# Performance work log

Measured on AMD Instinct MI355X. Metric: run time of the kernel, lower is better.

## Reference

```python
import jax, jax.numpy as jnp
import numpy as np

B, T, C, H = 4, 2048, 1024, 128

def setup_inputs() -> dict:
    key = jax.random.key(0)
    k1, k2, k3, k4 = jax.random.split(key, 4)
    x = jax.random.normal(k1, (B, T, C), dtype=jnp.float32)
    # nn.Linear(C, H, bias=False) weights, stored as [C, H] so y = x @ W
    scale = 1.0 / np.sqrt(C)
    Wq = jax.random.normal(k2, (C, H), dtype=jnp.float32) * scale
    Wk = jax.random.normal(k3, (C, H), dtype=jnp.float32) * scale
    Wv = jax.random.normal(k4, (C, H), dtype=jnp.float32) * scale
    mask = jnp.tril(jnp.ones((T, T), dtype=jnp.int32))  # causal mask
    return {"x": x, "Wq": Wq, "Wk": Wk, "Wv": Wv, "mask": mask}

def reference(x, Wq, Wk, Wv, mask):
    # x: [B,T,C]; projections to [B,T,H]
    q = jnp.einsum("btc,ch->bth", x, Wq)
    k = jnp.einsum("btc,ch->bth", x, Wk)
    v = jnp.einsum("btc,ch->bth", x, Wv)
    # NOTE: original scales by C**-0.5 (embedding dim), not head_size**-0.5
    inv_scale = x.shape[-1] ** (-0.5)
    scores = jnp.einsum("bth,bsh->bts", q, k) * inv_scale  # [B,T,T]
    scores = jnp.where(mask == 0, -jnp.inf, scores)
    weights = jax.nn.softmax(scores, axis=-1)
    # Dropout(0.1) is identity in eval mode
    return jnp.einsum("bts,bsh->bth", weights, v)  # [B,T,H]
```

## Files before the change

### kernel.cpp

```cpp
#include <hip/hip_runtime.h>
#include <hip/hip_bf16.h>
#include <cstdint>


typedef __bf16 bf16_t;
typedef __bf16 bf16x4 __attribute__((ext_vector_type(4)));
typedef __bf16 bf16x8 __attribute__((ext_vector_type(8)));
typedef float f32x4 __attribute__((ext_vector_type(4)));

#define MFMA16(a, b, c) __builtin_amdgcn_mfma_f32_16x16x32_bf16(a, b, c, 0, 0, 0)

constexpr int T = 2048;
constexpr int C = 1024;
constexpr int H = 128;
constexpr int BK = 64;

__device__ inline void gld16(const void* g, void* l) {
    __builtin_amdgcn_global_load_lds(
        (const __attribute__((address_space(1))) unsigned int*)g,
        (__attribute__((address_space(3))) unsigned int*)l, 16, 0, 0);
}

__global__ __launch_bounds__(256) void transpose_w(const float* __restrict__ Wq,
                                                   const float* __restrict__ Wk,
                                                   const float* __restrict__ Wv,
                                                   bf16_t* __restrict__ Wt) {
    __shared__ bf16_t tile[32][34];
    const int tid = threadIdx.x, blk = blockIdx.x;
    const int z = blk >> 7, rem = blk & 127;
    const int c0 = (rem & 31) * 32, h0 = (rem >> 5) * 32;
    const float* W = z == 0 ? Wq : (z == 1 ? Wk : Wv);
    const int tx = tid & 31, ty = tid >> 5;
#pragma unroll
    for (int i = 0; i < 4; i++)
        tile[ty + 8 * i][tx] = (bf16_t)W[(size_t)(c0 + ty + 8 * i) * H + h0 + tx];
    __syncthreads();
    bf16_t* Wtz = Wt + (size_t)z * H * C;
#pragma unroll
    for (int i = 0; i < 4; i++)
        Wtz[(size_t)(h0 + ty + 8 * i) * C + c0 + tx] = tile[tx][ty + 8 * i];
}

__global__ __launch_bounds__(256) void proj_gemm(const float* __restrict__ x,
                                                 const bf16_t* __restrict__ Wt,
                                                 bf16_t* __restrict__ qout,
                                                 bf16_t* __restrict__ kout,
                                                 bf16_t* __restrict__ vtout) {
    __shared__ __align__(16) float Ab[2][64 * BK];
    __shared__ __align__(16) bf16_t Bb[2][128 * BK];
    const int tid = threadIdx.x;
    const int w = tid >> 6, lane = tid & 63;
    const int m16 = lane & 15, g = lane >> 4;
    const int wm = w & 1, wn = w >> 1;
    const int z = blockIdx.y;
    const int m0 = blockIdx.x * 64;
    const bf16_t* Bsrc = Wt + (size_t)z * H * C;

    auto stage = [&](int s, int k0) {
#pragma unroll
        for (int i = 0; i < 4; i++) {
            const int e = i * 256 + tid;
            const int r = e >> 4, v = e & 15, c4 = v ^ (r & 15);
            gld16(x + (size_t)(m0 + r) * C + k0 + c4 * 4, &Ab[s][(i * 4 + w) * 256]);
        }
#pragma unroll
        for (int i = 0; i < 4; i++) {
            const int e = i * 256 + tid;
            const int r = e >> 3, v = e & 7, c8 = v ^ (r & 7);
            gld16(Bsrc + (size_t)r * C + k0 + c8 * 8, &Bb[s][(i * 4 + w) * 512]);
        }
    };

    f32x4 zero = {0.f, 0.f, 0.f, 0.f};
    f32x4 acc[2][4];
#pragma unroll
    for (int mf = 0; mf < 2; mf++)
#pragma unroll
        for (int nf = 0; nf < 4; nf++) acc[mf][nf] = zero;

    stage(0, 0);
    for (int c = 0; c < C / BK; c++) {
        __syncthreads();
        if (c + 1 < C / BK) stage((c + 1) & 1, (c + 1) * BK);
        const int s = c & 1;

        bf16x8 af[2][2], bfr[4][2];
#pragma unroll
        for (int mf = 0; mf < 2; mf++)
#pragma unroll
            for (int kf = 0; kf < 2; kf++) {
                const int r = wm * 32 + mf * 16 + m16;
                const int c4 = kf * 8 + g * 2;
                const int va = c4 ^ (r & 15), vb = (c4 + 1) ^ (r & 15);
                float4 fa = *(const float4*)(&Ab[s][r * BK + va * 4]);
                float4 fb = *(const float4*)(&Ab[s][r * BK + vb * 4]);
                bf16x8 t;
                t[0] = (bf16_t)fa.x; t[1] = (bf16_t)fa.y;
                t[2] = (bf16_t)fa.z; t[3] = (bf16_t)fa.w;
                t[4] = (bf16_t)fb.x; t[5] = (bf16_t)fb.y;
                t[6] = (bf16_t)fb.z; t[7] = (bf16_t)fb.w;
                af[mf][kf] = t;
            }
#pragma unroll
        for (int nf = 0; nf < 4; nf++)
#pragma unroll
            for (int kf = 0; kf < 2; kf++) {
                const int r = wn * 64 + nf * 16 + m16;
                const int v = (kf * 4 + g) ^ (r & 7);
                bfr[nf][kf] = *(const bf16x8*)(&Bb[s][r * BK + v * 8]);
            }
#pragma unroll
        for (int kf = 0; kf < 2; kf++)
#pragma unroll
            for (int mf = 0; mf < 2; mf++)
#pragma unroll
                for (int nf = 0; nf < 4; nf++)
                    acc[mf][nf] = MFMA16(af[mf][kf], bfr[nf][kf], acc[mf][nf]);
    }

    const float sc = (z == 0) ? 0.03125f : 1.0f;
    if (z < 2) {
        bf16_t* o = (z == 0) ? qout : kout;
#pragma unroll
        for (int mf = 0; mf < 2; mf++)
#pragma unroll
            for (int nf = 0; nf < 4; nf++)
#pragma unroll
                for (int ri = 0; ri < 4; ri++) {
                    const int r = m0 + wm * 32 + mf * 16 + g * 4 + ri;
                    const int n = wn * 64 + nf * 16 + m16;
                    o[(size_t)r * H + n] = (bf16_t)(acc[mf][nf][ri] * sc);
                }
    } else {
#pragma unroll
        for (int mf = 0; mf < 2; mf++) {
            const int t0 = m0 + wm * 32 + mf * 16 + g * 4;
            const int bidx = t0 >> 11, tt = t0 & (T - 1);
#pragma unroll
            for (int nf = 0; nf < 4; nf++) {
                const int h = wn * 64 + nf * 16 + m16;
                bf16x4 vv;
#pragma unroll
                for (int ri = 0; ri < 4; ri++) vv[ri] = (bf16_t)acc[mf][nf][ri];
                *(bf16x4*)(vtout + ((size_t)bidx * H + h) * T + tt) = vv;
            }
        }
    }
}

__global__ __launch_bounds__(512, 4) void attn(const bf16_t* __restrict__ q,
                                               const bf16_t* __restrict__ k,
                                               const bf16_t* __restrict__ vt,
                                               float* __restrict__ out) {
    __shared__ float buf[4][16][128];
    __shared__ __align__(16) bf16_t pbuf[8][16][40];
    __shared__ float mred[8][16], lred[8][16];
    const int tid = threadIdx.x;
    const int w = tid >> 6;
    const int lane = tid & 63;
    const int m16 = lane & 15, g = lane >> 4;
    const int b = blockIdx.x & 3;
    const int kk = blockIdx.x >> 2;
    const int qt = (kk < 64) ? kk : 191 - kk;
    const int q0 = qt * 16;

    const bf16_t* qb = q + (size_t)b * T * H;
    const bf16_t* kb = k + (size_t)b * T * H;
    const bf16_t* vb = vt + (size_t)b * H * T;

    bf16x8 aq[4];
#pragma unroll
    for (int c = 0; c < 4; c++)
        aq[c] = *(const bf16x8*)(qb + (size_t)(q0 + m16) * H + c * 32 + g * 8);

    bf16x8 ones;
#pragma unroll
    for (int i = 0; i < 8; i++) ones[i] = (bf16_t)1.0f;

    f32x4 zero = {0.f, 0.f, 0.f, 0.f};
    f32x4 acc[9];
#pragma unroll
    for (int ht = 0; ht < 9; ht++) acc[ht] = zero;
    float mst[4];
#pragma unroll
    for (int ri = 0; ri < 4; ri++) mst[ri] = -1e30f;

    const int kv_end = q0 + 16;
    bf16x8 kc[8], kn[8], vc[8];
    int kv0 = w * 32;
    if (kv0 < kv_end) {
#pragma unroll
        for (int t = 0; t < 2; t++)
#pragma unroll
            for (int c = 0; c < 4; c++)
                kc[t * 4 + c] = *(const bf16x8*)(kb + (size_t)(kv0 + t * 16 + m16) * H + c * 32 + g * 8);
    }

    for (; kv0 < kv_end; kv0 += 256) {
        f32x4 s[2];
        s[0] = zero; s[1] = zero;
#pragma unroll
        for (int t = 0; t < 2; t++)
#pragma unroll
            for (int c = 0; c < 4; c++)
                s[t] = MFMA16(aq[c], kc[t * 4 + c], s[t]);

#pragma unroll
        for (int ht = 0; ht < 8; ht++)
            vc[ht] = *(const bf16x8*)(vb + (size_t)(ht * 16 + m16) * T + kv0 + g * 8);

        const int kvn = kv0 + 256;
        if (kvn < kv_end) {
#pragma unroll
            for (int t = 0; t < 2; t++)
#pragma unroll
                for (int c = 0; c < 4; c++)
                    kn[t * 4 + c] = *(const bf16x8*)(kb + (size_t)(kvn + t * 16 + m16) * H + c * 32 + g * 8);
        }

        float p0v[4], p1v[4];
#pragma unroll
        for (int ri = 0; ri < 4; ri++) {
            const int row = q0 + g * 4 + ri;
            float v0 = s[0][ri];
            float v1 = s[1][ri];
            if (kv0 + m16 > row) v0 = -1e30f;
            if (kv0 + 16 + m16 > row) v1 = -1e30f;
            float rm = fmaxf(v0, v1);
#pragma unroll
            for (int off = 1; off < 16; off <<= 1) rm = fmaxf(rm, __shfl_xor(rm, off));
            const float mnew = fmaxf(mst[ri], rm);
            const float alpha = __expf(mst[ri] - mnew);
            mst[ri] = mnew;
            p0v[ri] = __expf(v0 - mnew);
            p1v[ri] = __expf(v1 - mnew);
#pragma unroll
            for (int ht = 0; ht < 9; ht++) acc[ht][ri] *= alpha;
        }

#pragma unroll
        for (int ri = 0; ri < 4; ri++) {
            pbuf[w][g * 4 + ri][m16] = (bf16_t)p0v[ri];
            pbuf[w][g * 4 + ri][16 + m16] = (bf16_t)p1v[ri];
        }
        bf16x8 ap = *(const bf16x8*)(&pbuf[w][m16][g * 8]);

#pragma unroll
        for (int ht = 0; ht < 8; ht++)
            acc[ht] = MFMA16(ap, vc[ht], acc[ht]);
        acc[8] = MFMA16(ap, ones, acc[8]);

#pragma unroll
        for (int i = 0; i < 8; i++) kc[i] = kn[i];
    }

    if (m16 == 0) {
#pragma unroll
        for (int ri = 0; ri < 4; ri++) mred[w][g * 4 + ri] = mst[ri];
    }
    __syncthreads();
    float scale[4];
#pragma unroll
    for (int ri = 0; ri < 4; ri++) {
        const int row = g * 4 + ri;
        float mt = mred[0][row];
#pragma unroll
        for (int j = 1; j < 8; j++) mt = fmaxf(mt, mred[j][row]);
        scale[ri] = __expf(mst[ri] - mt);
    }
    if (m16 == 0) {
#pragma unroll
        for (int ri = 0; ri < 4; ri++) lred[w][g * 4 + ri] = acc[8][ri] * scale[ri];
    }
#pragma unroll
    for (int ht = 0; ht < 8; ht++)
#pragma unroll
        for (int ri = 0; ri < 4; ri++) acc[ht][ri] *= scale[ri];

    if (w >= 4) {
#pragma unroll
        for (int ht = 0; ht < 8; ht++)
#pragma unroll
            for (int ri = 0; ri < 4; ri++)
                buf[w - 4][g * 4 + ri][ht * 16 + m16] = acc[ht][ri];
    }
    __syncthreads();
    if (w < 4) {
#pragma unroll
        for (int ht = 0; ht < 8; ht++)
#pragma unroll
            for (int ri = 0; ri < 4; ri++)
                acc[ht][ri] += buf[w][g * 4 + ri][ht * 16 + m16];
    }
    __syncthreads();
    if (w == 2 || w == 3) {
#pragma unroll
        for (int ht = 0; ht < 8; ht++)
#pragma unroll
            for (int ri = 0; ri < 4; ri++)
                buf[w - 2][g * 4 + ri][ht * 16 + m16] = acc[ht][ri];
    }
    __syncthreads();
    if (w < 2) {
#pragma unroll
        for (int ht = 0; ht < 8; ht++)
#pragma unroll
            for (int ri = 0; ri < 4; ri++)
                acc[ht][ri] += buf[w][g * 4 + ri][ht * 16 + m16];
    }
    __syncthreads();
    if (w == 1) {
#pragma unroll
        for (int ht = 0; ht < 8; ht++)
#pragma unroll
            for (int ri = 0; ri < 4; ri++)
                buf[1][g * 4 + ri][ht * 16 + m16] = acc[ht][ri];
    }
    __syncthreads();
    if (w == 0) {
        float* ob = out + ((size_t)b * T + q0) * H;
#pragma unroll
        for (int ri = 0; ri < 4; ri++) {
            const int row = g * 4 + ri;
            float lt = lred[0][row];
#pragma unroll
            for (int j = 1; j < 8; j++) lt += lred[j][row];
            const float inv = 1.f / lt;
#pragma unroll
            for (int ht = 0; ht < 8; ht++)
                ob[(size_t)row * H + ht * 16 + m16] =
                    (acc[ht][ri] + buf[1][row][ht * 16 + m16]) * inv;
        }
    }
}

extern "C" void kernel_launch(void* const* d_in, const int* in_sizes, int n_in,
                              void* d_out, int out_size, void* d_ws, size_t ws_size,
                              hipStream_t stream) {
    const float* x = (const float*)d_in[0];
    const float* Wq = (const float*)d_in[1];
    const float* Wk = (const float*)d_in[2];
    const float* Wv = (const float*)d_in[3];
    float* out = (float*)d_out;

    char* ws = (char*)d_ws;
    bf16_t* Wt = (bf16_t*)ws;
    char* p = ws + 786432;
    bf16_t* qb = (bf16_t*)(p);
    bf16_t* kb = (bf16_t*)(p + 2097152);
    bf16_t* vt = (bf16_t*)(p + 2 * 2097152);

    hipLaunchKernelGGL(transpose_w, dim3(384), dim3(256), 0, stream,
                       Wq, Wk, Wv, Wt);
    hipLaunchKernelGGL(proj_gemm, dim3(128, 3), dim3(256), 0, stream,
                       x, Wt, qb, kb, vt);
    hipLaunchKernelGGL(attn, dim3(512), dim3(512), 0, stream,
                       qb, kb, vt, out);
}
```

Measured before the change: 167.0 us.

## Pre-convert x to bf16, drop K prefetch, reorder attention tiles longest-first

A new prep kernel converts all of x to bf16 in one pass and also does the weight transpose, so proj_gemm stages bf16 tiles into LDS and no longer converts in its inner loop. That adds a 32MB read and 16MB write of x in exchange for halving the projection's A-operand load traffic. The attention kernel drops its register double-buffered K prefetch, changes launch bounds from 4 to 2 waves per SIMD, and schedules query tiles longest-first instead of the paired zig-zag order. Removing the prefetch may expose K load latency in the attention loop.

```diff
diff --git a/kernel.cpp b/kernel.cpp
--- a/kernel.cpp
+++ b/kernel.cpp
@@ -15,41 +15,60 @@
 constexpr int H = 128;
 constexpr int BK = 64;
 
+__device__ inline bf16x8 load8f(const float* __restrict__ p) {
+    float4 a = *(const float4*)p;
+    float4 b = *(const float4*)(p + 4);
+    bf16x8 r;
+    r[0] = (bf16_t)a.x; r[1] = (bf16_t)a.y; r[2] = (bf16_t)a.z; r[3] = (bf16_t)a.w;
+    r[4] = (bf16_t)b.x; r[5] = (bf16_t)b.y; r[6] = (bf16_t)b.z; r[7] = (bf16_t)b.w;
+    return r;
+}
+
 __device__ inline void gld16(const void* g, void* l) {
     __builtin_amdgcn_global_load_lds(
         (const __attribute__((address_space(1))) unsigned int*)g,
         (__attribute__((address_space(3))) unsigned int*)l, 16, 0, 0);
 }
 
-__global__ __launch_bounds__(256) void transpose_w(const float* __restrict__ Wq,
-                                                   const float* __restrict__ Wk,
-                                                   const float* __restrict__ Wv,
-                                                   bf16_t* __restrict__ Wt) {
-    __shared__ bf16_t tile[32][34];
-    const int tid = threadIdx.x, blk = blockIdx.x;
-    const int z = blk >> 7, rem = blk & 127;
-    const int c0 = (rem & 31) * 32, h0 = (rem >> 5) * 32;
-    const float* W = z == 0 ? Wq : (z == 1 ? Wk : Wv);
-    const int tx = tid & 31, ty = tid >> 5;
-#pragma unroll
-    for (int i = 0; i < 4; i++)
-        tile[ty + 8 * i][tx] = (bf16_t)W[(size_t)(c0 + ty + 8 * i) * H + h0 + tx];
-    __syncthreads();
-    bf16_t* Wtz = Wt + (size_t)z * H * C;
-#pragma unroll
-    for (int i = 0; i < 4; i++)
-        Wtz[(size_t)(h0 + ty + 8 * i) * C + c0 + tx] = tile[tx][ty + 8 * i];
-}
-
-__global__ __launch_bounds__(256) void proj_gemm(const float* __restrict__ x,
+__global__ __launch_bounds__(256) void prep(const float* __restrict__ x,
+                                            const float* __restrict__ Wq,
+                                            const float* __restrict__ Wk,
+                                            const float* __restrict__ Wv,
+                                            bf16_t* __restrict__ xb,
+                                            bf16_t* __restrict__ Wt) {
+    const int t = threadIdx.x;
+    if (blockIdx.x < 2048) {
+        const int n8 = 4 * T * C / 8;
+        int i = blockIdx.x * 256 + t;
+        for (; i < n8; i += 2048 * 256)
+            *(bf16x8*)(xb + (size_t)i * 8) = load8f(x + (size_t)i * 8);
+    } else {
+        __shared__ bf16_t tile[32][34];
+        const int b2 = blockIdx.x - 2048;
+        const int z = b2 >> 7, rem = b2 & 127;
+        const int c0 = (rem & 31) * 32, h0 = (rem >> 5) * 32;
+        const float* W = z == 0 ? Wq : (z == 1 ? Wk : Wv);
+        const int tx = t & 31, ty = t >> 5;
+#pragma unroll
+        for (int i = 0; i < 4; i++)
+            tile[ty + 8 * i][tx] = (bf16_t)W[(size_t)(c0 + ty + 8 * i) * H + h0 + tx];
+        __syncthreads();
+        bf16_t* Wtz = Wt + (size_t)z * H * C;
+#pragma unroll
+        for (int i = 0; i < 4; i++)
+            Wtz[(size_t)(h0 + ty + 8 * i) * C + c0 + tx] = tile[tx][ty + 8 * i];
+    }
+}
+
+__global__ __launch_bounds__(256) void proj_gemm(const bf16_t* __restrict__ xb,
                                                  const bf16_t* __restrict__ Wt,
                                                  bf16_t* __restrict__ qout,
                                                  bf16_t* __restrict__ kout,
                                                  bf16_t* __restrict__ vtout) {
-    __shared__ __align__(16) float Ab[2][64 * BK];
+    __shared__ __align__(16) bf16_t Ab[2][64 * BK];
     __shared__ __align__(16) bf16_t Bb[2][128 * BK];
-    const int tid = threadIdx.x;
-    const int w = tid >> 6, lane = tid & 63;
+    const int t = threadIdx.x;
+    const int w = t >> 6, lane = t & 63;
     const int m16 = lane & 15, g = lane >> 4;
     const int wm = w & 1, wn = w >> 1;
     const int z = blockIdx.y;
@@ -58,14 +77,14 @@
 
     auto stage = [&](int s, int k0) {
 #pragma unroll
+        for (int i = 0; i < 2; i++) {
+            const int e = i * 256 + t;
+            const int r = e >> 3, v = e & 7, c8 = v ^ (r & 7);
+            gld16(xb + (size_t)(m0 + r) * C + k0 + c8 * 8, &Ab[s][(i * 4 + w) * 512]);
+        }
+#pragma unroll
         for (int i = 0; i < 4; i++) {
-            const int e = i * 256 + tid;
-            const int r = e >> 4, v = e & 15, c4 = v ^ (r & 15);
-            gld16(x + (size_t)(m0 + r) * C + k0 + c4 * 4, &Ab[s][(i * 4 + w) * 256]);
-        }
-#pragma unroll
-        for (int i = 0; i < 4; i++) {
-            const int e = i * 256 + tid;
+            const int e = i * 256 + t;
             const int r = e >> 3, v = e & 7, c8 = v ^ (r & 7);
             gld16(Bsrc + (size_t)r * C + k0 + c8 * 8, &Bb[s][(i * 4 + w) * 512]);
         }
@@ -90,16 +109,8 @@
 #pragma unroll
             for (int kf = 0; kf < 2; kf++) {
                 const int r = wm * 32 + mf * 16 + m16;
-                const int c4 = kf * 8 + g * 2;
-                const int va = c4 ^ (r & 15), vb = (c4 + 1) ^ (r & 15);
-                float4 fa = *(const float4*)(&Ab[s][r * BK + va * 4]);
-                float4 fb = *(const float4*)(&Ab[s][r * BK + vb * 4]);
-                bf16x8 t;
-                t[0] = (bf16_t)fa.x; t[1] = (bf16_t)fa.y;
-                t[2] = (bf16_t)fa.z; t[3] = (bf16_t)fa.w;
-                t[4] = (bf16_t)fb.x; t[5] = (bf16_t)fb.y;
-                t[6] = (bf16_t)fb.z; t[7] = (bf16_t)fb.w;
-                af[mf][kf] = t;
+                const int v = (kf * 4 + g) ^ (r & 7);
+                af[mf][kf] = *(const bf16x8*)(&Ab[s][r * BK + v * 8]);
             }
 #pragma unroll
         for (int nf = 0; nf < 4; nf++)
@@ -148,7 +159,7 @@
     }
 }
 
-__global__ __launch_bounds__(512, 4) void attn(const bf16_t* __restrict__ q,
+__global__ __launch_bounds__(512, 2) void attn(const bf16_t* __restrict__ q,
                                                const bf16_t* __restrict__ k,
                                                const bf16_t* __restrict__ vt,
                                                float* __restrict__ out) {
@@ -161,7 +172,7 @@
     const int m16 = lane & 15, g = lane >> 4;
     const int b = blockIdx.x & 3;
     const int kk = blockIdx.x >> 2;
-    const int qt = (kk < 64) ? kk : 191 - kk;
+    const int qt = 127 - kk;
     const int q0 = qt * 16;
 
     const bf16_t* qb = q + (size_t)b * T * H;
@@ -186,17 +197,14 @@
     for (int ri = 0; ri < 4; ri++) mst[ri] = -1e30f;
 
     const int kv_end = q0 + 16;
-    bf16x8 kc[8], kn[8], vc[8];
-    int kv0 = w * 32;
-    if (kv0 < kv_end) {
+    for (int kv0 = w * 32; kv0 < kv_end; kv0 += 256) {
+        bf16x8 kc[8], vc[8];
 #pragma unroll
         for (int t = 0; t < 2; t++)
 #pragma unroll
             for (int c = 0; c < 4; c++)
                 kc[t * 4 + c] = *(const bf16x8*)(kb + (size_t)(kv0 + t * 16 + m16) * H + c * 32 + g * 8);
-    }
-
-    for (; kv0 < kv_end; kv0 += 256) {
+
         f32x4 s[2];
         s[0] = zero; s[1] = zero;
 #pragma unroll
@@ -208,15 +216,6 @@
 #pragma unroll
         for (int ht = 0; ht < 8; ht++)
             vc[ht] = *(const bf16x8*)(vb + (size_t)(ht * 16 + m16) * T + kv0 + g * 8);
-
-        const int kvn = kv0 + 256;
-        if (kvn < kv_end) {
-#pragma unroll
-            for (int t = 0; t < 2; t++)
-#pragma unroll
-                for (int c = 0; c < 4; c++)
-                    kn[t * 4 + c] = *(const bf16x8*)(kb + (size_t)(kvn + t * 16 + m16) * H + c * 32 + g * 8);
-        }
 
         float p0v[4], p1v[4];
 #pragma unroll
@@ -249,9 +248,6 @@
         for (int ht = 0; ht < 8; ht++)
             acc[ht] = MFMA16(ap, vc[ht], acc[ht]);
         acc[8] = MFMA16(ap, ones, acc[8]);
-
-#pragma unroll
-        for (int i = 0; i < 8; i++) kc[i] = kn[i];
     }
 
     if (m16 == 0) {
@@ -344,16 +340,17 @@
     float* out = (float*)d_out;
 
     char* ws = (char*)d_ws;
-    bf16_t* Wt = (bf16_t*)ws;
-    char* p = ws + 786432;
+    bf16_t* xb = (bf16_t*)ws;
+    bf16_t* Wt = (bf16_t*)(ws + 16777216);
+    char* p = ws + 16777216 + 786432;
     bf16_t* qb = (bf16_t*)(p);
     bf16_t* kb = (bf16_t*)(p + 2097152);
     bf16_t* vt = (bf16_t*)(p + 2 * 2097152);
 
-    hipLaunchKernelGGL(transpose_w, dim3(384), dim3(256), 0, stream,
-                       Wq, Wk, Wv, Wt);
+    hipLaunchKernelGGL(prep, dim3(2048 + 384), dim3(256), 0, stream,
+                       x, Wq, Wk, Wv, xb, Wt);
     hipLaunchKernelGGL(proj_gemm, dim3(128, 3), dim3(256), 0, stream,
-                       x, Wt, qb, kb, vt);
+                       xb, Wt, qb, kb, vt);
     hipLaunchKernelGGL(attn, dim3(512), dim3(512), 0, stream,
                        qb, kb, vt, out);
 }
```

Result: faster. 157.6 us (-5.6%).
